# Optimization experiments

Measured on AMD Instinct MI355X. Metric: run time of the kernel, lower is better.

## Reference

```python
import jax, jax.numpy as jnp
import numpy as np

L, K, C, D, E = 4, 3, 512, 512, 512   # layers, kwidth, channels, embed_dim, encoding_dim
T, B, S, V, MAXT = 1024, 16, 512, 32, 1024


def setup_inputs() -> dict:
    key = jax.random.key(0)
    ks = jax.random.split(key, 16)
    n = lambda k, sh, s=0.02: jax.random.normal(k, sh, dtype=jnp.float32) * s
    return {
        "labels": jax.random.randint(ks[0], (T, B), 0, V),
        "enc_seq": jax.random.uniform(ks[1], (S, B, E), dtype=jnp.float32),
        "label_embed_W": n(ks[2], (V, D)),
        "time_embed_W": n(ks[3], (MAXT, D)),
        "conv_glu_w": n(ks[4], (L, C, C, K)),
        "conv_glu_b": jnp.zeros((L, C), jnp.float32),
        "conv_id_w": n(ks[5], (L, C, C, K)),
        "conv_id_b": jnp.zeros((L, C), jnp.float32),
        "res_proj_w": n(ks[6], (L, C, C)),
        "res_proj_b": jnp.zeros((L, C), jnp.float32),
        "inres_w": n(ks[7], (L, C, D)),
        "inres_b": jnp.zeros((L, C), jnp.float32),
        "in2enc_w": n(ks[8], (L, E, C)),
        "in2enc_b": jnp.ones((L, E), jnp.float32),  # positive bias keeps sum-normalizer well conditioned
        "lab2enc_w": n(ks[9], (L, E, D)),
        "lab2enc_b": jnp.zeros((L, E), jnp.float32),
        "enc2in_w": n(ks[10], (L, C, E)),
        "enc2in_b": jnp.zeros((L, C), jnp.float32),
        "out_res_w": n(ks[11], (V, D)),
        "out_res_b": jnp.zeros((V,), jnp.float32),
        "out_proj_w": n(ks[12], (V, C)),
        "out_proj_b": jnp.zeros((V,), jnp.float32),
    }


def causal_conv(x, w, b):
    # x: (T, B, Cin); w: (Cout, Cin, K) -> left-padded (causal) conv, out (T, B, Cout)
    x_ = jnp.transpose(x, (1, 2, 0))  # (B, Cin, T)
    y = jax.lax.conv_general_dilated(
        x_, w, window_strides=(1,), padding=[(w.shape[-1] - 1, 0)],
        dimension_numbers=("NCH", "OIH", "NCH"))
    return jnp.transpose(y, (2, 0, 1)) + b


def reference(labels, enc_seq, label_embed_W, time_embed_W, conv_glu_w, conv_glu_b,
              conv_id_w, conv_id_b, res_proj_w, res_proj_b, inres_w, inres_b,
              in2enc_w, in2enc_b, lab2enc_w, lab2enc_b, enc2in_w, enc2in_b,
              out_res_w, out_res_b, out_proj_w, out_proj_b):
    Tn = labels.shape[0]
    emb = label_embed_W[labels] + time_embed_W[jnp.arange(Tn)][:, None, :]  # (T,B,D)
    h = emb
    for i in range(conv_glu_w.shape[0]):
        x = causal_conv(h, conv_glu_w[i], conv_glu_b[i])
        g = causal_conv(h, conv_id_w[i], conv_id_b[i])
        conv_out = (x * jax.nn.sigmoid(g)
                    + jnp.einsum('tbc,oc->tbo', h, res_proj_w[i]) + res_proj_b[i])
        # attention: dot-product scores normalized by their SUM over encoder axis (no softmax)
        d = (jnp.einsum('tbc,ec->tbe', conv_out, in2enc_w[i]) + in2enc_b[i]
             + jnp.einsum('tbd,ed->tbe', emb, lab2enc_w[i]) + lab2enc_b[i])
        raw = jnp.einsum('tbe,sbe->tsb', d, enc_seq)          # (T,S,B)
        attn = raw / jnp.sum(raw, axis=1, keepdims=True)
        ctx = jnp.einsum('tsb,sbe->tbe', attn, enc_seq)        # (T,B,E)
        ctx_proj = jnp.einsum('tbe,ce->tbc', ctx, enc2in_w[i]) + enc2in_b[i]
        h = conv_out + ctx_proj + jnp.einsum('tbd,cd->tbc', emb, inres_w[i]) + inres_b[i]
    out = (jnp.einsum('tbc,vc->tbv', h, out_proj_w) + out_proj_b
           + jnp.einsum('tbd,vd->tbv', emb, out_res_w) + out_res_b)
    return out
```

## Files before the change

kernel.cpp:

```cpp
#include <hip/hip_runtime.h>
#include <math.h>

#define Tn 1024
#define Bn 16
#define Sn 512
#define Vn 32
#define Cn 512
#define En 512
#define Ln 4
#define Kw 3
#define MROWS 16384
#define PADROWS 32
#define PADE (PADROWS * Cn)

typedef short bf16x8 __attribute__((ext_vector_type(8)));
typedef float f32x4 __attribute__((ext_vector_type(4)));

__device__ __forceinline__ unsigned short cvt_bf16(float x) {
  unsigned u = __builtin_bit_cast(unsigned, x);
  u = (u + 0x7FFFu + ((u >> 16) & 1u)) >> 16;
  return (unsigned short)u;
}
__device__ __forceinline__ float bf2f(unsigned short h) {
  unsigned u = ((unsigned)h) << 16;
  return __builtin_bit_cast(float, u);
}

#define GL16(g, l)                                                                     \
  __builtin_amdgcn_global_load_lds((const __attribute__((address_space(1))) void*)(g), \
                                   (__attribute__((address_space(3))) void*)(l), 16, 0, 0)

template <int N>
__device__ __forceinline__ void wait_vm_bar() {
  asm volatile("s_waitcnt vmcnt(%0)\n\ts_barrier" ::"i"(N) : "memory");
}
__device__ __forceinline__ void tail_bar() {
  asm volatile("s_waitcnt lgkmcnt(0)\n\ts_barrier" ::: "memory");
}

__device__ __forceinline__ const unsigned short* seg_sel(const unsigned short* s0,
                                                         const unsigned short* s1,
                                                         const unsigned short* s2, int q) {
  const unsigned short* r = s0;
  r = (q == 1) ? s1 : r;
  r = (q == 2) ? s2 : r;
  return r;
}

template <int EPI, int NKT>
__global__ __launch_bounds__(512, 4) void g2(
    const unsigned short* __restrict__ a0, const unsigned short* __restrict__ a1,
    const unsigned short* __restrict__ a2, int ald, size_t az,
    const unsigned short* __restrict__ b0, const unsigned short* __restrict__ b1,
    const unsigned short* __restrict__ b2, int bld, size_t bz,
    const float* __restrict__ bias, const unsigned short* __restrict__ addbf,
    const float* __restrict__ dden, unsigned short* __restrict__ out, int old_, size_t oz) {
  __shared__ char SA[32768], SB[32768];
  const int tid = threadIdx.x;
  const int lane = tid & 63, wave = tid >> 6;
  const int r15 = lane & 15;
  const int sq = ((lane >> 4) ^ ((r15 >> 1) & 3)) << 4;
  const int waveM = (wave >> 2) << 6;
  const int waveN = (wave & 3) << 5;
  const int m0 = blockIdx.x * 128, n0 = blockIdx.y * 128;
  const int z = blockIdx.z;
  const unsigned short* A0 = a0 + (size_t)z * az;
  const unsigned short* A1 = a1 + (size_t)z * az;
  const unsigned short* A2 = a2 + (size_t)z * az;
  const unsigned short* B0 = b0 + (size_t)z * bz;
  const unsigned short* B1 = b1 + (size_t)z * bz;
  const unsigned short* B2 = b2 + (size_t)z * bz;
  const int strow = tid >> 2;
  const int stcol = ((tid & 3) ^ ((tid >> 3) & 3)) << 3;
  const int lofs = tid * 16;
  f32x4 acc[4][2] = {};

#define STAGE_T(KT, SL)                                                                  \
  do {                                                                                   \
    const unsigned short* ab_ = seg_sel(A0, A1, A2, (KT) >> 3) +                         \
                                (size_t)(m0 + strow) * ald + (((KT) & 7) << 6) + stcol;  \
    const unsigned short* bb_ = seg_sel(B0, B1, B2, (KT) >> 3) +                         \
                                (size_t)(n0 + strow) * bld + (((KT) & 7) << 6) + stcol;  \
    GL16(ab_, SA + (SL) * 16384 + lofs);                                                 \
    GL16(ab_ + 32, SA + (SL) * 16384 + 8192 + lofs);                                     \
    GL16(bb_, SB + (SL) * 16384 + lofs);                                                 \
    GL16(bb_ + 32, SB + (SL) * 16384 + 8192 + lofs);                                     \
  } while (0)

  STAGE_T(0, 0);
  for (int kt = 0; kt < NKT; ++kt) {
    const int sl = kt & 1;
    if (kt + 1 < NKT) {
      STAGE_T(kt + 1, sl ^ 1);
      wait_vm_bar<4>();
    } else {
      wait_vm_bar<0>();
    }
    const char* abase = SA + sl * 16384 + (waveM + r15) * 64 + sq;
    const char* bbase = SB + sl * 16384 + (waveN + r15) * 64 + sq;
    __builtin_amdgcn_s_setprio(1);
#pragma unroll
    for (int kp = 0; kp < 2; ++kp) {
      bf16x8 af[4], bfv[2];
#pragma unroll
      for (int i = 0; i < 4; ++i) af[i] = *(const bf16x8*)(abase + kp * 8192 + i * 1024);
#pragma unroll
      for (int j = 0; j < 2; ++j) bfv[j] = *(const bf16x8*)(bbase + kp * 8192 + j * 1024);
#pragma unroll
      for (int i = 0; i < 4; ++i)
#pragma unroll
        for (int j = 0; j < 2; ++j)
          acc[i][j] = __builtin_amdgcn_mfma_f32_16x16x32_bf16(af[i], bfv[j], acc[i][j], 0, 0, 0);
    }
    __builtin_amdgcn_s_setprio(0);
    tail_bar();
  }
#undef STAGE_T

  const int q4 = (lane >> 4) << 2;
#pragma unroll
  for (int i = 0; i < 4; ++i) {
    int row = m0 + waveM + i * 16 + q4;
    if constexpr (EPI == 0) {
      int xcol = ((n0 + waveN) >> 1) + r15;
      float bx = bias[n0 + waveN + r15];
      float bg = bias[n0 + waveN + 16 + r15];
#pragma unroll
      for (int rr = 0; rr < 4; ++rr) {
        float xv = acc[i][0][rr] + bx;
        float gv = acc[i][1][rr] + bg;
        float sg = 1.f / (1.f + __expf(-gv));
        out[(size_t)(row + rr) * 512 + xcol] = cvt_bf16(xv * sg);
      }
    } else if constexpr (EPI == 3) {
#pragma unroll
      for (int rr = 0; rr < 4; ++rr) {
        float inv = 1.f / dden[z + (size_t)(row + rr) * 16];
#pragma unroll
        for (int j = 0; j < 2; ++j) {
          int col = n0 + waveN + j * 16 + r15;
          out[(size_t)z * oz + (size_t)(row + rr) * old_ + col] = cvt_bf16(acc[i][j][rr] * inv);
        }
      }
    } else {
#pragma unroll
      for (int j = 0; j < 2; ++j) {
        int col = n0 + waveN + j * 16 + r15;
        float bb = (EPI == 4) ? 0.f : bias[col];
#pragma unroll
        for (int rr = 0; rr < 4; ++rr) {
          size_t o = (size_t)z * oz + (size_t)(row + rr) * old_ + col;
          float v = acc[i][j][rr] + bb;
          if constexpr (EPI == 2) v += bf2f(addbf[o]);
          out[o] = cvt_bf16(v);
        }
      }
    }
  }
}

__global__ __launch_bounds__(256, 4) void k_outm(const unsigned short* __restrict__ hd,
                                                 const unsigned short* __restrict__ embd,
                                                 const unsigned short* __restrict__ wcat2,
                                                 const float* __restrict__ bcat2,
                                                 float* __restrict__ out) {
  __shared__ char SA[32768];
  __shared__ char SBo[8192];
  const int tid = threadIdx.x;
  const int lane = tid & 63, wave = tid >> 6;
  const int r15 = lane & 15;
  const int sq = ((lane >> 4) ^ ((r15 >> 1) & 3)) << 4;
  const int waveM = wave << 5;
  const int m0 = blockIdx.x * 128;
  f32x4 acc[2][2] = {};
  const int aru = ((tid & 255) + 0);
  (void)aru;

#define OSTAGE(KT, SL)                                                                         \
  do {                                                                                         \
    const unsigned short* aseg = ((KT) < 8) ? hd : embd;                                       \
    int kc = ((KT) & 7) << 6;                                                                  \
    _Pragma("unroll") for (int q = 0; q < 2; ++q) {                                            \
      int unit = q * 256 + tid;                                                                \
      int row = unit >> 2, chunk = unit & 3;                                                   \
      int swc = chunk ^ ((row >> 1) & 3);                                                      \
      GL16(aseg + (size_t)(m0 + row) * 512 + kc + swc * 8, SA + (SL) * 16384 + unit * 16);     \
      GL16(aseg + (size_t)(m0 + row) * 512 + kc + 32 + swc * 8,                                \
           SA + (SL) * 16384 + 8192 + unit * 16);                                              \
    }                                                                                          \
    {                                                                                          \
      int half = tid >> 7;                                                                     \
      int u = tid & 127;                                                                       \
      int row = u >> 2, chunk = u & 3;                                                         \
      int swc = chunk ^ ((row >> 1) & 3);                                                      \
      GL16(wcat2 + (size_t)row * 1024 + ((KT) << 6) + half * 32 + swc * 8,                     \
           SBo + (SL) * 4096 + half * 2048 + u * 16);                                          \
    }                                                                                          \
  } while (0)

  OSTAGE(0, 0);
  for (int kt = 0; kt < 16; ++kt) {
    const int sl = kt & 1;
    if (kt + 1 < 16) {
      OSTAGE(kt + 1, sl ^ 1);
      wait_vm_bar<5>();
    } else {
      wait_vm_bar<0>();
    }
    const char* abase = SA + sl * 16384 + (waveM + r15) * 64 + sq;
    const char* bbase = SBo + sl * 4096 + r15 * 64 + sq;
    __builtin_amdgcn_s_setprio(1);
#pragma unroll
    for (int kp = 0; kp < 2; ++kp) {
      bf16x8 af[2], bfv[2];
#pragma unroll
      for (int i = 0; i < 2; ++i) af[i] = *(const bf16x8*)(abase + kp * 8192 + i * 1024);
#pragma unroll
      for (int j = 0; j < 2; ++j) bfv[j] = *(const bf16x8*)(bbase + kp * 2048 + j * 1024);
#pragma unroll
      for (int i = 0; i < 2; ++i)
#pragma unroll
        for (int j = 0; j < 2; ++j)
          acc[i][j] = __builtin_amdgcn_mfma_f32_16x16x32_bf16(af[i], bfv[j], acc[i][j], 0, 0, 0);
    }
    __builtin_amdgcn_s_setprio(0);
    tail_bar();
  }
#undef OSTAGE

  const int q4 = (lane >> 4) << 2;
#pragma unroll
  for (int i = 0; i < 2; ++i) {
    int row = m0 + waveM + i * 16 + q4;
#pragma unroll
    for (int j = 0; j < 2; ++j) {
      int col = j * 16 + r15;
      float bb = bcat2[col];
#pragma unroll
      for (int rr = 0; rr < 4; ++rr)
        out[(size_t)(row + rr) * 32 + col] = acc[i][j][rr] + bb;
    }
  }
}


__global__ __launch_bounds__(256) void emb_kernel(const int* __restrict__ labels,
                                                  const float* __restrict__ labW,
                                                  const float* __restrict__ timeW,
                                                  unsigned short* __restrict__ embd) {
  int idx = blockIdx.x * 256 + threadIdx.x;
  int dd = idx & 511;
  int m = idx >> 9;
  int t = m >> 4;
  embd[idx] = cvt_bf16(labW[labels[m] * 512 + dd] + timeW[t * 512 + dd]);
}

__global__ void k_zeropad(unsigned short* a, unsigned short* b, unsigned short* c) {
  int i = blockIdx.x * 256 + threadIdx.x;
  a[i] = 0; b[i] = 0; c[i] = 0;
}

__global__ void k_wcat(const float* __restrict__ wx, const float* __restrict__ wg,
                       unsigned short* __restrict__ wcat) {
  int idx = blockIdx.x * 256 + threadIdx.x;
  int k = idx % 1536;
  int tmp = idx / 1536;
  int orow = tmp & 1023;
  int l = tmp >> 10;
  int tap = k >> 9, c = k & 511;
  int q = orow >> 5, r = orow & 31;
  int srow = q * 16 + (r & 15);
  const float* src = (r < 16) ? wx : wg;
  float v = src[(((size_t)l * 512 + srow) * 512 + c) * 3 + tap];
  wcat[idx] = cvt_bf16(v);
}

__global__ void k_biascat(const float* __restrict__ bx, const float* __restrict__ bg,
                          float* __restrict__ bcat) {
  int idx = blockIdx.x * 256 + threadIdx.x;
  int orow = idx & 1023, l = idx >> 10;
  int q = orow >> 5, r = orow & 31;
  bcat[idx] = (r < 16) ? bx[l * 512 + q * 16 + r] : bg[l * 512 + q * 16 + (r & 15)];
}

__global__ void k_wcat2(const float* __restrict__ opw, const float* __restrict__ orw,
                        const float* __restrict__ opb, const float* __restrict__ orb,
                        unsigned short* __restrict__ wcat2, float* __restrict__ bcat2) {
  int idx = blockIdx.x * 256 + threadIdx.x;
  int v = idx >> 10, k = idx & 1023;
  float val = (k < 512) ? opw[v * 512 + k] : orw[v * 512 + k - 512];
  wcat2[idx] = cvt_bf16(val);
  if (idx < 32) bcat2[idx] = opb[idx] + orb[idx];
}

__global__ void cast_kernel(const float* __restrict__ src, unsigned short* __restrict__ dst,
                            int n) {
  int i = blockIdx.x * 256 + threadIdx.x;
  if (i < n) dst[i] = cvt_bf16(src[i]);
}

__global__ __launch_bounds__(256) void k_tr512(const float* __restrict__ w,
                                               unsigned short* __restrict__ wt) {
  __shared__ unsigned short t[64][65];
  int r0 = blockIdx.x * 64, c0 = blockIdx.y * 64;
  size_t base = (size_t)blockIdx.z * 512 * 512;
  int c = threadIdx.x & 63, rr = threadIdx.x >> 6;
#pragma unroll
  for (int i = 0; i < 16; ++i) {
    int r = rr + i * 4;
    t[r][c] = cvt_bf16(w[base + (size_t)(r0 + r) * 512 + c0 + c]);
  }
  __syncthreads();
#pragma unroll
  for (int i = 0; i < 16; ++i) {
    int r = rr + i * 4;
    wt[base + (size_t)(c0 + r) * 512 + r0 + c] = t[c][r];
  }
}

__global__ void esum_kernel(const float* __restrict__ enc, float* __restrict__ Esum) {
  int p = blockIdx.x * 256 + threadIdx.x;
  float s = 0.f;
  for (int ss = 0; ss < Sn; ++ss) s += enc[(size_t)ss * Bn * En + p];
  Esum[p] = s;
}

__global__ __launch_bounds__(256) void k_encT(const float* __restrict__ enc,
                                              unsigned short* __restrict__ encT) {
  __shared__ unsigned short t[64][66];
  int s0 = blockIdx.x * 64, e0 = blockIdx.y * 64, b = blockIdx.z;
  int c = threadIdx.x & 63, r0 = threadIdx.x >> 6;
#pragma unroll
  for (int i = 0; i < 16; ++i) {
    int r = r0 + i * 4;
    t[r][c] = cvt_bf16(enc[((size_t)(s0 + r) * Bn + b) * En + e0 + c]);
  }
  __syncthreads();
#pragma unroll
  for (int i = 0; i < 16; ++i) {
    int r = r0 + i * 4;
    encT[((size_t)b * En + e0 + r) * Sn + s0 + c] = t[c][r];
  }
}

__global__ void k_biasprep(const float* __restrict__ i2e, const float* __restrict__ res_b,
                           const float* __restrict__ in2enc_b, const float* __restrict__ lab2enc_b,
                           const float* __restrict__ e2i_b, const float* __restrict__ inres_b,
                           float* __restrict__ bd, float* __restrict__ bh) {
  int idx = blockIdx.x * 256 + threadIdx.x;
  int l = idx >> 9;
  float v = 0.f;
  const float* row = i2e + (size_t)idx * 512;
  const float* rb = res_b + l * 512;
  for (int c = 0; c < 512; ++c) v += row[c] * rb[c];
  bd[idx] = v + in2enc_b[idx] + lab2enc_b[idx];
  bh[idx] = res_b[idx] + e2i_b[idx] + inres_b[idx];
}

__global__ __launch_bounds__(256) void den_kernel(const unsigned short* __restrict__ d,
                                                  const float* __restrict__ Esum,
                                                  float* __restrict__ den) {
  int gtid = blockIdx.x * 256 + threadIdx.x;
  int row = gtid >> 6;
  int lane = threadIdx.x & 63;
  int b = row & 15;
  const unsigned short* dp = d + (size_t)row * 512 + lane * 8;
  const float* ep = Esum + b * 512 + lane * 8;
  float s = 0.f;
#pragma unroll
  for (int q = 0; q < 8; ++q) s += bf2f(dp[q]) * ep[q];
  for (int off = 32; off; off >>= 1) s += __shfl_down(s, off, 64);
  if (lane == 0) den[row] = s;
}


extern "C" void kernel_launch(void* const* d_in, const int* in_sizes, int n_in,
                              void* d_out, int out_size, void* d_ws, size_t ws_size,
                              hipStream_t stream) {
  const int* labels = (const int*)d_in[0];
  const float* enc = (const float*)d_in[1];
  const float* labW = (const float*)d_in[2];
  const float* timeW = (const float*)d_in[3];
  const float* conv_glu_w = (const float*)d_in[4];
  const float* conv_glu_b = (const float*)d_in[5];
  const float* conv_id_w = (const float*)d_in[6];
  const float* conv_id_b = (const float*)d_in[7];
  const float* res_proj_w = (const float*)d_in[8];
  const float* res_proj_b = (const float*)d_in[9];
  const float* inres_w = (const float*)d_in[10];
  const float* inres_b = (const float*)d_in[11];
  const float* in2enc_w = (const float*)d_in[12];
  const float* in2enc_b = (const float*)d_in[13];
  const float* lab2enc_w = (const float*)d_in[14];
  const float* lab2enc_b = (const float*)d_in[15];
  const float* enc2in_w = (const float*)d_in[16];
  const float* enc2in_b = (const float*)d_in[17];
  const float* out_res_w = (const float*)d_in[18];
  const float* out_res_b = (const float*)d_in[19];
  const float* out_proj_w = (const float*)d_in[20];
  const float* out_proj_b = (const float*)d_in[21];
  float* out = (float*)d_out;

  char* cur = (char*)d_ws;
  auto alloc = [&](size_t bytes) {
    char* p = cur;
    cur += (bytes + 255) & ~(size_t)255;
    return p;
  };
  const size_t BIG = (size_t)MROWS * 512;
  const size_t WN = (size_t)Ln * Cn * Cn;
  const size_t ZL = (size_t)512 * 512;
  float* den = (float*)alloc(MROWS * 4);
  float* EsumB = (float*)alloc(Bn * En * 4);
  float* bd = (float*)alloc(Ln * 512 * 4);
  float* bh = (float*)alloc(Ln * 512 * 4);
  float* bcat = (float*)alloc(Ln * 1024 * 4);
  float* bcat2 = (float*)alloc(32 * 4);
  unsigned short* embp = (unsigned short*)alloc((PADE + BIG) * 2);
  unsigned short* h0p = (unsigned short*)alloc((PADE + BIG) * 2);
  unsigned short* h1p = (unsigned short*)alloc((PADE + BIG) * 2);
  unsigned short* glubf = (unsigned short*)alloc(BIG * 2);
  unsigned short* dbf = (unsigned short*)alloc(BIG * 2);
  unsigned short* ctxbf = (unsigned short*)alloc(BIG * 2);
  unsigned short* encT = (unsigned short*)alloc((size_t)Bn * En * Sn * 2);
  unsigned short* Mbf = (unsigned short*)alloc((size_t)Bn * En * En * 2);
  unsigned short* wres = (unsigned short*)alloc(WN * 2);
  unsigned short* resT = (unsigned short*)alloc(WN * 2);
  unsigned short* wfuse = (unsigned short*)alloc(WN * 2);
  unsigned short* wcat = (unsigned short*)alloc((size_t)Ln * 1024 * 1536 * 2);
  unsigned short* wcat2 = (unsigned short*)alloc((size_t)32 * 1024 * 2);
  unsigned short* w_i2e = (unsigned short*)alloc(WN * 2);
  unsigned short* w_l2e = (unsigned short*)alloc(WN * 2);
  unsigned short* w_inr = (unsigned short*)alloc(WN * 2);
  unsigned short* w_e2i = (unsigned short*)alloc(WN * 2);

  unsigned short* embd = embp + PADE;
  unsigned short* h0d = h0p + PADE;
  unsigned short* h1d = h1p + PADE;

  emb_kernel<<<MROWS * 512 / 256, 256, 0, stream>>>(labels, labW, timeW, embd);
  k_zeropad<<<PADE / 256, 256, 0, stream>>>(embp, h0p, h1p);
  k_wcat<<<Ln * 1024 * 1536 / 256, 256, 0, stream>>>(conv_glu_w, conv_id_w, wcat);
  k_biascat<<<Ln * 1024 / 256, 256, 0, stream>>>(conv_glu_b, conv_id_b, bcat);
  k_wcat2<<<32 * 1024 / 256, 256, 0, stream>>>(out_proj_w, out_res_w, out_proj_b, out_res_b,
                                               wcat2, bcat2);
  cast_kernel<<<WN / 256, 256, 0, stream>>>(res_proj_w, wres, WN);
  cast_kernel<<<WN / 256, 256, 0, stream>>>(in2enc_w, w_i2e, WN);
  cast_kernel<<<WN / 256, 256, 0, stream>>>(lab2enc_w, w_l2e, WN);
  cast_kernel<<<WN / 256, 256, 0, stream>>>(inres_w, w_inr, WN);
  cast_kernel<<<WN / 256, 256, 0, stream>>>(enc2in_w, w_e2i, WN);
  k_tr512<<<dim3(8, 8, Ln), 256, 0, stream>>>(res_proj_w, resT);
  k_biasprep<<<Ln * 512 / 256, 256, 0, stream>>>(in2enc_w, res_proj_b, in2enc_b, lab2enc_b,
                                                 enc2in_b, inres_b, bd, bh);
  esum_kernel<<<Bn * En / 256, 256, 0, stream>>>(enc, EsumB);
  k_encT<<<dim3(Sn / 64, En / 64, Bn), 256, 0, stream>>>(enc, encT);
  g2<4, 8><<<dim3(4, 4, Bn), 512, 0, stream>>>(encT, encT, encT, Sn, ZL, encT, encT, encT, Sn,
                                               ZL, nullptr, nullptr, nullptr, Mbf, 512, ZL);
  g2<4, 8><<<dim3(4, 4, Ln), 512, 0, stream>>>(w_i2e, w_i2e, w_i2e, 512, ZL, resT, resT, resT,
                                               512, ZL, nullptr, nullptr, nullptr, wfuse, 512, ZL);

  const unsigned short* hdata = embd;
  unsigned short* hbufs[2] = {h0d, h1d};
  for (int l = 0; l < Ln; ++l) {
    const size_t wo = (size_t)l * Cn * Cn;
    const unsigned short* wc = wcat + (size_t)l * 1024 * 1536;
    g2<0, 24><<<dim3(128, 8), 512, 0, stream>>>(
        hdata - 2 * Bn * 512, hdata - Bn * 512, hdata, 512, 0, wc, wc + 512, wc + 1024, 1536, 0,
        bcat + l * 1024, nullptr, nullptr, glubf, 512, 0);
    g2<1, 24><<<dim3(128, 4), 512, 0, stream>>>(
        glubf, hdata, embd, 512, 0, w_i2e + wo, wfuse + wo, w_l2e + wo, 512, 0, bd + l * 512,
        nullptr, nullptr, dbf, 512, 0);
    den_kernel<<<MROWS / 4, 256, 0, stream>>>(dbf, EsumB, den);
    g2<3, 8><<<dim3(8, 4, Bn), 512, 0, stream>>>(dbf, dbf, dbf, 8192, 512, Mbf, Mbf, Mbf, 512,
                                                 ZL, nullptr, nullptr, den, ctxbf, 8192, 512);
    g2<2, 24><<<dim3(128, 4), 512, 0, stream>>>(
        hdata, ctxbf, embd, 512, 0, wres + wo, w_e2i + wo, w_inr + wo, 512, 0, bh + l * 512,
        glubf, nullptr, hbufs[l & 1], 512, 0);
    hdata = hbufs[l & 1];
  }

  k_outm<<<MROWS / 128, 256, 0, stream>>>(hdata, embd, wcat2, bcat2, out);
}
```

Before: 669.4 us.

## Replace per-layer GEMMs with larger-tile kernels using staggered load/compute pipelining

Adds two new GEMM kernels for the big per-layer products. g3glu uses 256x256 tiles for the conv+GLU GEMM, and g3t uses 256x128 tiles for the projection GEMMs, each with 64-byte-row XOR-swizzled LDS. Global-to-LDS loads for the next K step are split into chunks and interleaved between MFMA groups, with partial vmcnt waits. The goal is more data reuse per block and better overlap of memory traffic with compute. The cost is higher register and LDS use (launch bounds 2 blocks per CU) and fewer blocks in the grid, so fewer waves are available to hide latency.

```diff
diff --git a/kernel.cpp b/kernel.cpp
--- a/kernel.cpp
+++ b/kernel.cpp
@@ -37,6 +37,11 @@
 __device__ __forceinline__ void tail_bar() {
   asm volatile("s_waitcnt lgkmcnt(0)\n\ts_barrier" ::: "memory");
 }
+#define VMB(N)                                                   \
+  do {                                                           \
+    asm volatile("s_waitcnt vmcnt(%0)" ::"i"(N) : "memory");     \
+    __builtin_amdgcn_s_barrier();                                \
+  } while (0)
 
 __device__ __forceinline__ const unsigned short* seg_sel(const unsigned short* s0,
                                                          const unsigned short* s1,
@@ -45,6 +50,224 @@
   r = (q == 1) ? s1 : r;
   r = (q == 2) ? s2 : r;
   return r;
+}
+
+__global__ __launch_bounds__(512, 2) void g3glu(const unsigned short* __restrict__ hd,
+                                                const unsigned short* __restrict__ wc,
+                                                const float* __restrict__ bias,
+                                                unsigned short* __restrict__ out) {
+  __shared__ char LA[2][32768];
+  __shared__ char LB[2][32768];
+  const int tid = threadIdx.x;
+  const int lane = tid & 63;
+  const int wm = (tid >> 6) >> 2;
+  const int wn = (tid >> 6) & 3;
+  const int r15 = lane & 15;
+  const int l4 = lane >> 4;
+  const int q4 = l4 << 2;
+  const int m0 = blockIdx.x * 256, n0 = blockIdx.y * 256;
+  const int srow = tid >> 3;
+  const int scol = (((tid & 7) ^ (srow & 7)) << 3);
+  const int sdst = tid << 4;
+  f32x4 acc[8][4] = {};
+  bf16x8 afr[4][2], b01[2][2], b23[2][2];
+  const unsigned short* hs0 = hd - 2 * 16 * 512;
+  const unsigned short* hs1 = hd - 16 * 512;
+
+#define SGA3(KT, H, BB)                                                                     \
+  do {                                                                                      \
+    const unsigned short* s_ = seg_sel(hs0, hs1, hd, (KT) >> 3) +                           \
+                               (size_t)(m0 + (H) * 128 + srow) * 512 + (((KT)&7) << 6) +    \
+                               scol;                                                        \
+    GL16(s_, LA[BB] + (H) * 16384 + sdst);                                                  \
+    GL16(s_ + (size_t)64 * 512, LA[BB] + (H) * 16384 + 8192 + sdst);                        \
+  } while (0)
+#define SGB3(KT, H, BB)                                                                     \
+  do {                                                                                      \
+    const unsigned short* s_ =                                                              \
+        wc + (size_t)(n0 + (H) * 128 + srow) * 1536 + ((KT) << 6) + scol;                   \
+    GL16(s_, LB[BB] + (H) * 16384 + sdst);                                                  \
+    GL16(s_ + (size_t)64 * 1536, LB[BB] + (H) * 16384 + 8192 + sdst);                       \
+  } while (0)
+#define RDA3(SL, FH)                                                                        \
+  do {                                                                                      \
+    _Pragma("unroll") for (int f = 0; f < 4; ++f) _Pragma("unroll") for (int kp = 0;        \
+                                                                         kp < 2; ++kp) {   \
+      int ar = ((FH) << 7) + (wm << 6) + (f << 4) + r15;                                    \
+      afr[f][kp] =                                                                          \
+          *(const bf16x8*)(LA[SL] + ar * 128 + ((((kp << 2) | l4) ^ (ar & 7)) << 4));       \
+    }                                                                                       \
+  } while (0)
+#define RDB3(SL, CH, DST)                                                                   \
+  do {                                                                                      \
+    _Pragma("unroll") for (int c = 0; c < 2; ++c) _Pragma("unroll") for (int kp = 0;        \
+                                                                         kp < 2; ++kp) {   \
+      int br = ((CH) << 7) + (wn << 5) + (c << 4) + r15;                                    \
+      DST[c][kp] =                                                                          \
+          *(const bf16x8*)(LB[SL] + br * 128 + ((((kp << 2) | l4) ^ (br & 7)) << 4));       \
+    }                                                                                       \
+  } while (0)
+#define MM3(BF, F0, C0)                                                                     \
+  do {                                                                                      \
+    __builtin_amdgcn_s_setprio(1);                                                          \
+    _Pragma("unroll") for (int f = 0; f < 4; ++f) _Pragma("unroll") for (int c = 0; c < 2;  \
+                                                                         ++c)              \
+        _Pragma("unroll") for (int kp = 0; kp < 2; ++kp) acc[(F0) + f][(C0) + c] =          \
+            __builtin_amdgcn_mfma_f32_16x16x32_bf16(afr[f][kp], BF[c][kp],                  \
+                                                    acc[(F0) + f][(C0) + c], 0, 0, 0);      \
+    __builtin_amdgcn_s_setprio(0);                                                          \
+  } while (0)
+#define GRP3(KT, W1, W2, W3, STG)                                                           \
+  do {                                                                                      \
+    const int sl_ = (KT)&1, sn_ = sl_ ^ 1;                                                  \
+    if (STG) SGA3((KT) + 1, 0, sn_);                                                        \
+    VMB(W1);                                                                                \
+    RDA3(sl_, 0);                                                                           \
+    RDB3(sl_, 0, b01);                                                                      \
+    MM3(b01, 0, 0);                                                                         \
+    if (STG) SGB3((KT) + 1, 0, sn_);                                                        \
+    VMB(W2);                                                                                \
+    RDB3(sl_, 1, b23);                                                                      \
+    MM3(b23, 0, 2);                                                                         \
+    if (STG) SGB3((KT) + 1, 1, sn_);                                                        \
+    VMB(W3);                                                                                \
+    RDA3(sl_, 1);                                                                           \
+    MM3(b23, 4, 2);                                                                         \
+    if (STG) SGA3((KT) + 1, 1, sn_);                                                        \
+    MM3(b01, 4, 0);                                                                         \
+  } while (0)
+
+  SGA3(0, 0, 0);
+  SGB3(0, 0, 0);
+  SGB3(0, 1, 0);
+  SGA3(0, 1, 0);
+  for (int kt = 0; kt < 23; ++kt) GRP3(kt, 6, 6, 6, 1);
+  GRP3(23, 4, 2, 0, 0);
+#undef GRP3
+
+#pragma unroll
+  for (int f = 0; f < 8; ++f) {
+    int grow = m0 + ((f >> 2) << 7) + (wm << 6) + ((f & 3) << 4) + q4;
+#pragma unroll
+    for (int p = 0; p < 2; ++p) {
+      int bcol = n0 + (p << 7) + (wn << 5);
+      float bx = bias[bcol + r15];
+      float bg = bias[bcol + 16 + r15];
+      int xcol = (bcol >> 1) + r15;
+#pragma unroll
+      for (int rr = 0; rr < 4; ++rr) {
+        float xv = acc[f][2 * p][rr] + bx;
+        float gv = acc[f][2 * p + 1][rr] + bg;
+        float sg = 1.f / (1.f + __expf(-gv));
+        out[(size_t)(grow + rr) * 512 + xcol] = cvt_bf16(xv * sg);
+      }
+    }
+  }
+}
+
+template <int EPI>
+__global__ __launch_bounds__(512, 2) void g3t(
+    const unsigned short* __restrict__ a0, const unsigned short* __restrict__ a1,
+    const unsigned short* __restrict__ a2, const unsigned short* __restrict__ b0,
+    const unsigned short* __restrict__ b1, const unsigned short* __restrict__ b2,
+    const float* __restrict__ bias, const unsigned short* __restrict__ addbf,
+    unsigned short* __restrict__ out) {
+  __shared__ char LA[2][32768];
+  __shared__ char LB[2][16384];
+  const int tid = threadIdx.x;
+  const int lane = tid & 63;
+  const int wm = (tid >> 6) >> 1;
+  const int wn = (tid >> 6) & 1;
+  const int r15 = lane & 15;
+  const int l4 = lane >> 4;
+  const int q4 = l4 << 2;
+  const int m0 = blockIdx.x * 256, n0 = blockIdx.y * 128;
+  const int srow = tid >> 3;
+  const int scol = (((tid & 7) ^ (srow & 7)) << 3);
+  const int sdst = tid << 4;
+  f32x4 acc[4][4] = {};
+  bf16x8 afr[4][2], b01[2][2], b23[2][2];
+
+#define TGA(KT, BB)                                                                         \
+  do {                                                                                      \
+    const unsigned short* s_ = seg_sel(a0, a1, a2, (KT) >> 3) +                             \
+                               (size_t)(m0 + srow) * 512 + (((KT)&7) << 6) + scol;          \
+    GL16(s_, LA[BB] + sdst);                                                                \
+    GL16(s_ + (size_t)64 * 512, LA[BB] + 8192 + sdst);                                      \
+    GL16(s_ + (size_t)128 * 512, LA[BB] + 16384 + sdst);                                    \
+    GL16(s_ + (size_t)192 * 512, LA[BB] + 24576 + sdst);                                    \
+  } while (0)
+#define TGB(KT, BB)                                                                         \
+  do {                                                                                      \
+    const unsigned short* s_ = seg_sel(b0, b1, b2, (KT) >> 3) +                             \
+                               (size_t)(n0 + srow) * 512 + (((KT)&7) << 6) + scol;          \
+    GL16(s_, LB[BB] + sdst);                                                                \
+    GL16(s_ + (size_t)64 * 512, LB[BB] + 8192 + sdst);                                      \
+  } while (0)
+#define TRA(SL)                                                                             \
+  do {                                                                                      \
+    _Pragma("unroll") for (int f = 0; f < 4; ++f) _Pragma("unroll") for (int kp = 0;        \
+                                                                         kp < 2; ++kp) {   \
+      int ar = ((f >> 1) << 7) + (wm << 5) + ((f & 1) << 4) + r15;                          \
+      afr[f][kp] =                                                                          \
+          *(const bf16x8*)(LA[SL] + ar * 128 + ((((kp << 2) | l4) ^ (ar & 7)) << 4));       \
+    }                                                                                       \
+  } while (0)
+#define TRB(SL, CH, DST)                                                                    \
+  do {                                                                                      \
+    _Pragma("unroll") for (int c = 0; c < 2; ++c) _Pragma("unroll") for (int kp = 0;        \
+                                                                         kp < 2; ++kp) {   \
+      int br = ((CH) << 6) + (wn << 5) + (c << 4) + r15;                                    \
+      DST[c][kp] =                                                                          \
+          *(const bf16x8*)(LB[SL] + br * 128 + ((((kp << 2) | l4) ^ (br & 7)) << 4));       \
+    }                                                                                       \
+  } while (0)
+#define MMT(BF, C0)                                                                         \
+  do {                                                                                      \
+    __builtin_amdgcn_s_setprio(1);                                                          \
+    _Pragma("unroll") for (int f = 0; f < 4; ++f) _Pragma("unroll") for (int c = 0; c < 2;  \
+                                                                         ++c)              \
+        _Pragma("unroll") for (int kp = 0; kp < 2; ++kp) acc[f][(C0) + c] =                 \
+            __builtin_amdgcn_mfma_f32_16x16x32_bf16(afr[f][kp], BF[c][kp],                  \
+                                                    acc[f][(C0) + c], 0, 0, 0);             \
+    __builtin_amdgcn_s_setprio(0);                                                          \
+  } while (0)
+#define TGRP(KT, W1, W2, STG)                                                               \
+  do {                                                                                      \
+    const int sl_ = (KT)&1, sn_ = sl_ ^ 1;                                                  \
+    if (STG) TGA((KT) + 1, sn_);                                                            \
+    VMB(W1);                                                                                \
+    TRA(sl_);                                                                               \
+    TRB(sl_, 0, b01);                                                                       \
+    MMT(b01, 0);                                                                            \
+    if (STG) TGB((KT) + 1, sn_);                                                            \
+    VMB(W2);                                                                                \
+    TRB(sl_, 1, b23);                                                                       \
+    MMT(b23, 2);                                                                            \
+  } while (0)
+
+  TGA(0, 0);
+  TGB(0, 0);
+  for (int kt = 0; kt < 23; ++kt) TGRP(kt, 5, 6, 1);
+  TGRP(23, 1, 0, 0);
+#undef TGRP
+
+#pragma unroll
+  for (int f = 0; f < 4; ++f) {
+    int grow = m0 + ((f >> 1) << 7) + (wm << 5) + ((f & 1) << 4) + q4;
+#pragma unroll
+    for (int c = 0; c < 4; ++c) {
+      int gcol = n0 + ((c >> 1) << 6) + (wn << 5) + ((c & 1) << 4) + r15;
+      float bb = bias[gcol];
+#pragma unroll
+      for (int rr = 0; rr < 4; ++rr) {
+        size_t o = (size_t)(grow + rr) * 512 + gcol;
+        float v = acc[f][c][rr] + bb;
+        if constexpr (EPI == 2) v += bf2f(addbf[o]);
+        out[o] = cvt_bf16(v);
+      }
+    }
+  }
 }
 
 template <int EPI, int NKT>
@@ -75,16 +298,16 @@
   const int lofs = tid * 16;
   f32x4 acc[4][2] = {};
 
-#define STAGE_T(KT, SL)                                                                  \
-  do {                                                                                   \
-    const unsigned short* ab_ = seg_sel(A0, A1, A2, (KT) >> 3) +                         \
-                                (size_t)(m0 + strow) * ald + (((KT) & 7) << 6) + stcol;  \
-    const unsigned short* bb_ = seg_sel(B0, B1, B2, (KT) >> 3) +                         \
-                                (size_t)(n0 + strow) * bld + (((KT) & 7) << 6) + stcol;  \
-    GL16(ab_, SA + (SL) * 16384 + lofs);                                                 \
-    GL16(ab_ + 32, SA + (SL) * 16384 + 8192 + lofs);                                     \
-    GL16(bb_, SB + (SL) * 16384 + lofs);                                                 \
-    GL16(bb_ + 32, SB + (SL) * 16384 + 8192 + lofs);                                     \
+#define STAGE_T(KT, SL)                                                                 \
+  do {                                                                                  \
+    const unsigned short* ab_ = seg_sel(A0, A1, A2, (KT) >> 3) +                        \
+                                (size_t)(m0 + strow) * ald + (((KT)&7) << 6) + stcol;   \
+    const unsigned short* bb_ = seg_sel(B0, B1, B2, (KT) >> 3) +                        \
+                                (size_t)(n0 + strow) * bld + (((KT)&7) << 6) + stcol;   \
+    GL16(ab_, SA + (SL)*16384 + lofs);                                                  \
+    GL16(ab_ + 32, SA + (SL)*16384 + 8192 + lofs);                                      \
+    GL16(bb_, SB + (SL)*16384 + lofs);                                                  \
+    GL16(bb_ + 32, SB + (SL)*16384 + 8192 + lofs);                                      \
   } while (0)
 
   STAGE_T(0, 0);
@@ -121,18 +344,7 @@
 #pragma unroll
   for (int i = 0; i < 4; ++i) {
     int row = m0 + waveM + i * 16 + q4;
-    if constexpr (EPI == 0) {
-      int xcol = ((n0 + waveN) >> 1) + r15;
-      float bx = bias[n0 + waveN + r15];
-      float bg = bias[n0 + waveN + 16 + r15];
-#pragma unroll
-      for (int rr = 0; rr < 4; ++rr) {
-        float xv = acc[i][0][rr] + bx;
-        float gv = acc[i][1][rr] + bg;
-        float sg = 1.f / (1.f + __expf(-gv));
-        out[(size_t)(row + rr) * 512 + xcol] = cvt_bf16(xv * sg);
-      }
-    } else if constexpr (EPI == 3) {
+    if constexpr (EPI == 3) {
 #pragma unroll
       for (int rr = 0; rr < 4; ++rr) {
         float inv = 1.f / dden[z + (size_t)(row + rr) * 16];
@@ -173,29 +385,27 @@
   const int waveM = wave << 5;
   const int m0 = blockIdx.x * 128;
   f32x4 acc[2][2] = {};
-  const int aru = ((tid & 255) + 0);
-  (void)aru;
-
-#define OSTAGE(KT, SL)                                                                         \
-  do {                                                                                         \
-    const unsigned short* aseg = ((KT) < 8) ? hd : embd;                                       \
-    int kc = ((KT) & 7) << 6;                                                                  \
-    _Pragma("unroll") for (int q = 0; q < 2; ++q) {                                            \
-      int unit = q * 256 + tid;                                                                \
-      int row = unit >> 2, chunk = unit & 3;                                                   \
-      int swc = chunk ^ ((row >> 1) & 3);                                                      \
-      GL16(aseg + (size_t)(m0 + row) * 512 + kc + swc * 8, SA + (SL) * 16384 + unit * 16);     \
-      GL16(aseg + (size_t)(m0 + row) * 512 + kc + 32 + swc * 8,                                \
-           SA + (SL) * 16384 + 8192 + unit * 16);                                              \
-    }                                                                                          \
-    {                                                                                          \
-      int half = tid >> 7;                                                                     \
-      int u = tid & 127;                                                                       \
-      int row = u >> 2, chunk = u & 3;                                                         \
-      int swc = chunk ^ ((row >> 1) & 3);                                                      \
-      GL16(wcat2 + (size_t)row * 1024 + ((KT) << 6) + half * 32 + swc * 8,                     \
-           SBo + (SL) * 4096 + half * 2048 + u * 16);                                          \
-    }                                                                                          \
+
+#define OSTAGE(KT, SL)                                                                     \
+  do {                                                                                     \
+    const unsigned short* aseg = ((KT) < 8) ? hd : embd;                                   \
+    int kc = ((KT)&7) << 6;                                                                \
+    _Pragma("unroll") for (int q = 0; q < 2; ++q) {                                        \
+      int unit = q * 256 + tid;                                                            \
+      int row = unit >> 2, chunk = unit & 3;                                               \
+      int swc = chunk ^ ((row >> 1) & 3);                                                  \
+      GL16(aseg + (size_t)(m0 + row) * 512 + kc + swc * 8, SA + (SL)*16384 + unit * 16);   \
+      GL16(aseg + (size_t)(m0 + row) * 512 + kc + 32 + swc * 8,                            \
+           SA + (SL)*16384 + 8192 + unit * 16);                                            \
+    }                                                                                      \
+    {                                                                                      \
+      int half = tid >> 7;                                                                 \
+      int u = tid & 127;                                                                   \
+      int row = u >> 2, chunk = u & 3;                                                     \
+      int swc = chunk ^ ((row >> 1) & 3);                                                  \
+      GL16(wcat2 + (size_t)row * 1024 + ((KT) << 6) + half * 32 + swc * 8,                 \
+           SBo + (SL)*4096 + half * 2048 + u * 16);                                        \
+    }                                                                                      \
   } while (0)
 
   OSTAGE(0, 0);
@@ -237,8 +447,7 @@
       int col = j * 16 + r15;
       float bb = bcat2[col];
 #pragma unroll
-      for (int rr = 0; rr < 4; ++rr)
-        out[(size_t)(row + rr) * 32 + col] = acc[i][j][rr] + bb;
+      for (int rr = 0; rr < 4; ++rr) out[(size_t)(row + rr) * 32 + col] = acc[i][j][rr] + bb;
     }
   }
 }
@@ -464,18 +673,14 @@
   for (int l = 0; l < Ln; ++l) {
     const size_t wo = (size_t)l * Cn * Cn;
     const unsigned short* wc = wcat + (size_t)l * 1024 * 1536;
-    g2<0, 24><<<dim3(128, 8), 512, 0, stream>>>(
-        hdata - 2 * Bn * 512, hdata - Bn * 512, hdata, 512, 0, wc, wc + 512, wc + 1024, 1536, 0,
-        bcat + l * 1024, nullptr, nullptr, glubf, 512, 0);
-    g2<1, 24><<<dim3(128, 4), 512, 0, stream>>>(
-        glubf, hdata, embd, 512, 0, w_i2e + wo, wfuse + wo, w_l2e + wo, 512, 0, bd + l * 512,
-        nullptr, nullptr, dbf, 512, 0);
+    g3glu<<<dim3(64, 4), 512, 0, stream>>>(hdata, wc, bcat + l * 1024, glubf);
+    g3t<1><<<dim3(64, 4), 512, 0, stream>>>(glubf, hdata, embd, w_i2e + wo, wfuse + wo,
+                                            w_l2e + wo, bd + l * 512, nullptr, dbf);
     den_kernel<<<MROWS / 4, 256, 0, stream>>>(dbf, EsumB, den);
     g2<3, 8><<<dim3(8, 4, Bn), 512, 0, stream>>>(dbf, dbf, dbf, 8192, 512, Mbf, Mbf, Mbf, 512,
                                                  ZL, nullptr, nullptr, den, ctxbf, 8192, 512);
-    g2<2, 24><<<dim3(128, 4), 512, 0, stream>>>(
-        hdata, ctxbf, embd, 512, 0, wres + wo, w_e2i + wo, w_inr + wo, 512, 0, bh + l * 512,
-        glubf, nullptr, hbufs[l & 1], 512, 0);
+    g3t<2><<<dim3(64, 4), 512, 0, stream>>>(hdata, ctxbf, embd, wres + wo, w_e2i + wo,
+                                            w_inr + wo, bh + l * 512, glubf, hbufs[l & 1]);
     hdata = hbufs[l & 1];
   }
 
```

After: 661.0 us. No clear change (-1.3%).
